# Performance work log

Measured on AMD Instinct MI355X. Metric: run time of the kernel, lower is better.

The kernel has to match this reference:

```python
import jax, jax.numpy as jnp
import numpy as np

B, S, D, H = 2, 2048, 2048, 16
HD = D // H            # 128
BLK = 16               # sparsity block size
LOCAL = 4              # num_local_blocks
GLOBAL = 1             # num_global_blocks
ROPE_THETA = 10000.0


def _fixed_layout(num_blocks: int) -> np.ndarray:
    """DeepSpeed FixedSparsityConfig block layout (unidirectional,
    different_layout_per_head=False, num_different_global_patterns=1,
    horizontal_global_attention=False)."""
    layout = np.zeros((num_blocks, num_blocks), dtype=bool)
    # local windows of LOCAL blocks, causal at block granularity inside window
    for w in range(0, num_blocks, LOCAL):
        end = min(w + LOCAL, num_blocks)
        for row in range(w, end):
            layout[row, w:row + 1] = True
    # vertical global columns: last GLOBAL block(s) of each window
    first = LOCAL - GLOBAL  # head % num_different_global_patterns == 0
    stop = num_blocks - (num_blocks % LOCAL)
    for i in range(first, stop, LOCAL):
        layout[i:, i:i + GLOBAL] = True  # unidirectional: rows >= i
    return layout

_LAYOUT = _fixed_layout(S // BLK)  # [num_blocks, num_blocks] bool, static


def _rope(t, cos, sin):
    # t: [B, S, H, HD]; pairs are adjacent (llama complex view)
    tr = t.reshape(B, S, H, HD // 2, 2)
    a, b = tr[..., 0], tr[..., 1]
    c = cos[None, :, None, :]
    s = sin[None, :, None, :]
    out = jnp.stack([a * c - b * s, a * s + b * c], axis=-1)
    return out.reshape(B, S, H, HD)


def setup_inputs() -> dict:
    key = jax.random.key(0)
    kx, kq, kk, kv, ko = jax.random.split(key, 5)
    x = jax.random.normal(kx, (B, S, D), dtype=jnp.float32)
    wscale = 1.0 / np.sqrt(D)
    wq = jax.random.normal(kq, (D, D), dtype=jnp.float32) * wscale
    wk = jax.random.normal(kk, (D, D), dtype=jnp.float32) * wscale
    wv = jax.random.normal(kv, (D, D), dtype=jnp.float32) * wscale
    wo = jax.random.normal(ko, (D, D), dtype=jnp.float32) * wscale
    # rotary tables (freqs_cis split into real/imag parts)
    freqs = 1.0 / (ROPE_THETA ** (np.arange(0, HD, 2, dtype=np.float32) / HD))
    angles = np.arange(S, dtype=np.float32)[:, None] * freqs[None, :]  # [S, HD//2]
    cos = jnp.asarray(np.cos(angles), dtype=jnp.float32)
    sin = jnp.asarray(np.sin(angles), dtype=jnp.float32)
    return {"x": x, "cos": cos, "sin": sin, "wq": wq, "wk": wk, "wv": wv, "wo": wo}


def reference(x, cos, sin, wq, wk, wv, wo):
    xq = (x @ wq).reshape(B, S, H, HD)
    xk = (x @ wk).reshape(B, S, H, HD)
    xv = (x @ wv).reshape(B, S, H, HD)
    xq = _rope(xq, cos, sin)
    xk = _rope(xk, cos, sin)
    # module casts q/k/v to fp16 before the sparse kernel; emulate precision
    xq = xq.astype(jnp.float16).astype(jnp.float32)
    xk = xk.astype(jnp.float16).astype(jnp.float32)
    xv = xv.astype(jnp.float16).astype(jnp.float32)
    q = jnp.transpose(xq, (0, 2, 1, 3))  # [B, H, S, HD]
    k = jnp.transpose(xk, (0, 2, 1, 3))
    v = jnp.transpose(xv, (0, 2, 1, 3))
    scale = 1.0 / np.sqrt(HD)
    scores = jnp.einsum('bhqd,bhkd->bhqk', q, k) * scale
    # block-granularity sparsity mask (DeepSpeed masks only at block level)
    blk = jnp.arange(S) // BLK
    mask = jnp.asarray(_LAYOUT)[blk[:, None], blk[None, :]]  # [S, S] bool
    scores = jnp.where(mask[None, None], scores, -jnp.inf)
    probs = jax.nn.softmax(scores, axis=-1)
    out = jnp.einsum('bhqk,bhkd->bhqd', probs, v)  # [B, H, S, HD]
    out = jnp.transpose(out, (0, 2, 1, 3)).reshape(B, S, D)
    return out @ wo
```

## Files before the change

### kernel.cpp

```cpp
#include <hip/hip_runtime.h>

#define B_ 2
#define S_ 2048
#define D_ 2048
#define H_ 16
#define HD_ 128

typedef _Float16 fp16x2 __attribute__((ext_vector_type(2)));
typedef _Float16 fp16x4 __attribute__((ext_vector_type(4)));
typedef _Float16 fp16x8 __attribute__((ext_vector_type(8)));
typedef float f32x4 __attribute__((ext_vector_type(4)));

__device__ __forceinline__ void gl_lds16(const _Float16* g, _Float16* l) {
  __builtin_amdgcn_global_load_lds((const __attribute__((address_space(1))) void*)g,
                                   (__attribute__((address_space(3))) void*)l, 16, 0, 0);
}

__global__ __launch_bounds__(256) void k_cast(const float* __restrict__ in,
                                              _Float16* __restrict__ out, int n4) {
  int i = blockIdx.x * 256 + threadIdx.x;
  if (i >= n4) return;
  f32x4 v = ((const f32x4*)in)[i];
  fp16x4 h = {(_Float16)v[0], (_Float16)v[1], (_Float16)v[2], (_Float16)v[3]};
  ((fp16x4*)out)[i] = h;
}

__global__ __launch_bounds__(256) void k_trw4(const float* __restrict__ w0,
                                              const float* __restrict__ w1,
                                              const float* __restrict__ w2,
                                              const float* __restrict__ w3,
                                              _Float16* __restrict__ o0,
                                              _Float16* __restrict__ o1,
                                              _Float16* __restrict__ o2,
                                              _Float16* __restrict__ o3) {
  __shared__ float tile[64][65];
  const float* w = (blockIdx.z == 0) ? w0 : (blockIdx.z == 1) ? w1 : (blockIdx.z == 2) ? w2 : w3;
  _Float16* wt = (blockIdx.z == 0) ? o0 : (blockIdx.z == 1) ? o1 : (blockIdx.z == 2) ? o2 : o3;
  int k0 = blockIdx.y * 64, n0 = blockIdx.x * 64;
  int t = threadIdx.x;
  int r = t >> 2, c0 = (t & 3) * 16;
  const float* ip = w + (size_t)(k0 + r) * D_ + n0 + c0;
#pragma unroll
  for (int j = 0; j < 16; j += 4) {
    f32x4 v = *(const f32x4*)(ip + j);
    tile[r][c0 + j] = v[0]; tile[r][c0 + j + 1] = v[1];
    tile[r][c0 + j + 2] = v[2]; tile[r][c0 + j + 3] = v[3];
  }
  __syncthreads();
  _Float16* op = wt + (size_t)(n0 + r) * D_ + k0 + c0;
#pragma unroll
  for (int j = 0; j < 16; j += 8) {
    fp16x8 v;
#pragma unroll
    for (int q = 0; q < 8; ++q) v[q] = (_Float16)tile[c0 + j + q][r];
    *(fp16x8*)(op + j) = v;
  }
}

__global__ __launch_bounds__(256, 4) void k_gemm_qkv(const _Float16* __restrict__ A,
                                                     const _Float16* __restrict__ BT,
                                                     const float* __restrict__ cosT,
                                                     const float* __restrict__ sinT,
                                                     _Float16* __restrict__ Qo,
                                                     _Float16* __restrict__ Ko,
                                                     _Float16* __restrict__ Vo) {
  __shared__ __align__(16) _Float16 lA[128 * 64];
  __shared__ __align__(16) _Float16 lB[128 * 64];
  const int t = threadIdx.x;
  const int fid = blockIdx.y * 48 + blockIdx.x;
  const int xcd = fid & 7, j = fid >> 3;
  const int m0 = (j / 6) * 128;
  const int n0 = (xcd * 6 + j % 6) * 128;
  const int lane = t & 63, w = t >> 6;
  const int l15 = lane & 15, lg = lane >> 4;
  const int wm = (w >> 1) * 64, wn = (w & 1) * 64;
  const int rs = t >> 3, cs = (t & 7) * 8;
  const _Float16* Ag = A + (size_t)(m0 + rs) * 2048 + cs;
  const _Float16* Bg = BT + (size_t)(n0 + rs) * 2048 + cs;
  _Float16* lAw = lA + w * 512;
  _Float16* lBw = lB + w * 512;
  f32x4 acc[4][4] = {};
  for (int k0 = 0; k0 < 2048; k0 += 64) {
#pragma unroll
    for (int i = 0; i < 4; ++i) {
      gl_lds16(Ag + k0 + (size_t)i * 32 * 2048, lAw + i * 2048);
      gl_lds16(Bg + k0 + (size_t)i * 32 * 2048, lBw + i * 2048);
    }
    __syncthreads();
#pragma unroll
    for (int ks = 0; ks < 2; ++ks) {
      const int ko = ks * 32 + 8 * lg;
      fp16x8 af[4], bf[4];
#pragma unroll
      for (int mi = 0; mi < 4; ++mi)
        af[mi] = *(const fp16x8*)&lA[(wm + mi * 16 + l15) * 64 + ko];
#pragma unroll
      for (int ni = 0; ni < 4; ++ni)
        bf[ni] = *(const fp16x8*)&lB[(wn + ni * 16 + l15) * 64 + ko];
#pragma unroll
      for (int mi = 0; mi < 4; ++mi)
#pragma unroll
        for (int ni = 0; ni < 4; ++ni)
          acc[mi][ni] = __builtin_amdgcn_mfma_f32_16x16x32_f16(af[mi], bf[ni], acc[mi][ni], 0, 0, 0);
    }
    __syncthreads();
  }

  const int region = n0 >> 11;
  if (region < 2) {
    _Float16* Out = (region == 0) ? Qo : Ko;
#pragma unroll
    for (int mi = 0; mi < 4; ++mi)
#pragma unroll
      for (int ni = 0; ni < 4; ++ni) {
        const int col = n0 + wn + 16 * ni + l15;
        const int d = col & 127;
        const int h = (col >> 7) & 15;
        const int dp = d >> 1;
        const bool odd = d & 1;
#pragma unroll
        for (int i = 0; i < 4; ++i) {
          const int row = m0 + wm + 16 * mi + 4 * lg + i;
          const int b = row >> 11, sl = row & 2047;
          const float self = acc[mi][ni][i];
          const float partner = __shfl_xor(self, 1);
          const float c = cosT[sl * 64 + dp], sn = sinT[sl * 64 + dp];
          const float val = odd ? (partner * sn + self * c) : (self * c - partner * sn);
          Out[(((size_t)b * H_ + h) * S_ + sl) * HD_ + d] = (_Float16)val;
        }
      }
  } else {
#pragma unroll
    for (int mi = 0; mi < 4; ++mi)
#pragma unroll
      for (int ni = 0; ni < 4; ++ni) {
        const int col = n0 + wn + 16 * ni + l15;
        const int d = col & 127;
        const int h = (col >> 7) & 15;
        const int row0 = m0 + wm + 16 * mi + 4 * lg;
        const int b = row0 >> 11, sl0 = row0 & 2047;
        const int kb = sl0 >> 4, kin = sl0 & 15;
        fp16x4 v4;
#pragma unroll
        for (int i = 0; i < 4; ++i) v4[i] = (_Float16)acc[mi][ni][i];
        *(fp16x4*)(Vo + ((((size_t)b * H_ + h) * 128 + kb) * 128 + d) * 16 + kin) = v4;
      }
  }
}

template <typename OUT>
__global__ __launch_bounds__(256) void k_gemm_bt(const _Float16* __restrict__ A,
                                                 const _Float16* __restrict__ BT,
                                                 OUT* __restrict__ C, int N) {
  __shared__ __align__(16) _Float16 lA[128 * 64];
  __shared__ __align__(16) _Float16 lB[128 * 64];
  const int t = threadIdx.x;
  const int fid = blockIdx.y * 16 + blockIdx.x;
  const int xcd = fid & 7, j = fid >> 3;
  const int m0 = (j >> 1) * 128;
  const int n0 = (xcd * 2 + (j & 1)) * 128;
  const int lane = t & 63, w = t >> 6;
  const int l15 = lane & 15, lg = lane >> 4;
  const int wm = (w >> 1) * 64, wn = (w & 1) * 64;
  const int rs = t >> 3, cs = (t & 7) * 8;
  const _Float16* Ag = A + (size_t)(m0 + rs) * 2048 + cs;
  const _Float16* Bg = BT + (size_t)(n0 + rs) * 2048 + cs;
  _Float16* lAw = lA + w * 512;
  _Float16* lBw = lB + w * 512;
  f32x4 acc[4][4] = {};
  for (int k0 = 0; k0 < 2048; k0 += 64) {
#pragma unroll
    for (int i = 0; i < 4; ++i) {
      gl_lds16(Ag + k0 + (size_t)i * 32 * 2048, lAw + i * 2048);
      gl_lds16(Bg + k0 + (size_t)i * 32 * 2048, lBw + i * 2048);
    }
    __syncthreads();
#pragma unroll
    for (int ks = 0; ks < 2; ++ks) {
      const int ko = ks * 32 + 8 * lg;
      fp16x8 af[4], bf[4];
#pragma unroll
      for (int mi = 0; mi < 4; ++mi)
        af[mi] = *(const fp16x8*)&lA[(wm + mi * 16 + l15) * 64 + ko];
#pragma unroll
      for (int ni = 0; ni < 4; ++ni)
        bf[ni] = *(const fp16x8*)&lB[(wn + ni * 16 + l15) * 64 + ko];
#pragma unroll
      for (int mi = 0; mi < 4; ++mi)
#pragma unroll
        for (int ni = 0; ni < 4; ++ni)
          acc[mi][ni] = __builtin_amdgcn_mfma_f32_16x16x32_f16(af[mi], bf[ni], acc[mi][ni], 0, 0, 0);
    }
    __syncthreads();
  }
#pragma unroll
  for (int mi = 0; mi < 4; ++mi)
#pragma unroll
    for (int ni = 0; ni < 4; ++ni) {
      size_t row = m0 + wm + 16 * mi + 4 * lg;
      size_t col = n0 + wn + 16 * ni + l15;
#pragma unroll
      for (int i = 0; i < 4; ++i)
        C[(row + i) * (size_t)N + col] = (OUT)acc[mi][ni][i];
    }
}

__global__ __launch_bounds__(256) void k_attn(const _Float16* __restrict__ Q,
                                              const _Float16* __restrict__ K,
                                              const _Float16* __restrict__ Vb,
                                              _Float16* __restrict__ Oa) {
  __shared__ __align__(16) _Float16 sK[2][2][2048];
  __shared__ __align__(16) _Float16 sV[2][2][2048];
  const int p = blockIdx.x;
  const int qgA = 31 - p, qgB = p;
  const int hh = blockIdx.y, b = blockIdx.z;
  const int t = threadIdx.x;
  const int w = t >> 6, lane = t & 63;
  const int l15 = lane & 15, lg = lane >> 4, g4 = lg * 4;
  const size_t bh = (size_t)b * H_ + hh;
  const float scale = 0.08838834764831845f;

  const int qbA = 4 * qgA + w, qbB = 4 * qgB + w;
  const int LA = qgA + 4, LB = qgB + 4;
  const int nchA = (LA + 1) >> 1, nchB = (LB + 1) >> 1;
  const int total = nchA + nchB;

  const _Float16* QpA = Q + (bh * S_ + (size_t)qbA * 16 + l15) * HD_ + lg * 8;
  const _Float16* QpB = Q + (bh * S_ + (size_t)qbB * 16 + l15) * HD_ + lg * 8;
  fp16x8 qfA[4], qfB[4];
#pragma unroll
  for (int dd = 0; dd < 4; ++dd) {
    qfA[dd] = *(const fp16x8*)(QpA + dd * 32);
    qfB[dd] = *(const fp16x8*)(QpB + dd * 32);
  }
  f32x4 o[8] = {};
  float mrun = -3.0e38f, lsum = 0.f;

  const int sr = t >> 4, sc = t & 15;
  const int ksrc_off = sr * 128 + (sc ^ (sr & 7)) * 8;
  const _Float16* Kb_g = K + bh * S_ * HD_;
  const _Float16* Vb_g = Vb + bh * (size_t)(128 * 2048);

  auto kbof = [&](int qg, int idx) { return idx < qg ? 4 * idx + 3 : 3 * qg + idx; };
  auto chunk_kbs = [&](int ci, int& kb0, int& kb1) {
    int qg, cil;
    if (ci < nchA) { qg = qgA; cil = ci; } else { qg = qgB; cil = ci - nchA; }
    const int L = qg + 4;
    const int i0 = 2 * cil, i1 = i0 + 1;
    kb0 = kbof(qg, i0);
    kb1 = (i1 < L) ? kbof(qg, i1) : kb0;
  };
  auto stage = [&](int buf, int ci) {
    int kb0, kb1;
    chunk_kbs(ci, kb0, kb1);
    gl_lds16(Kb_g + (size_t)kb0 * 2048 + ksrc_off, &sK[buf][0][w * 512]);
    gl_lds16(Kb_g + (size_t)kb1 * 2048 + ksrc_off, &sK[buf][1][w * 512]);
    gl_lds16(Vb_g + (size_t)kb0 * 2048 + t * 8, &sV[buf][0][w * 512]);
    gl_lds16(Vb_g + (size_t)kb1 * 2048 + t * 8, &sV[buf][1][w * 512]);
  };
  auto flush = [&](int qb) {
    const float inv = 1.f / lsum;
    f32x4 li;
#pragma unroll
    for (int i = 0; i < 4; ++i) li[i] = __shfl(inv, g4 + i);
    _Float16* Op = Oa + ((size_t)b * S_ + (size_t)qb * 16 + g4) * D_ + (size_t)hh * HD_ + l15;
#pragma unroll
    for (int ni = 0; ni < 8; ++ni)
#pragma unroll
      for (int i = 0; i < 4; ++i)
        Op[(size_t)i * D_ + 16 * ni] = (_Float16)(o[ni][i] * li[i]);
  };

  stage(0, 0);

  for (int ci = 0; ci < total; ++ci) {
    const int cur = ci & 1;
    if (ci == nchA) {
      flush(qbA);
#pragma unroll
      for (int ni = 0; ni < 8; ++ni) o[ni] = f32x4{0.f, 0.f, 0.f, 0.f};
      mrun = -3.0e38f;
      lsum = 0.f;
    }
    if (ci + 1 < total) {
      stage(cur ^ 1, ci + 1);
      asm volatile("s_waitcnt vmcnt(4)" ::: "memory");
    } else {
      asm volatile("s_waitcnt vmcnt(0)" ::: "memory");
    }
    __builtin_amdgcn_s_barrier();

    const bool inA = ci < nchA;
    const int qg = inA ? qgA : qgB;
    const int qb = inA ? qbA : qbB;
    const int cil = inA ? ci : ci - nchA;
    const int L = qg + 4;
    int kb0, kb1;
    chunk_kbs(ci, kb0, kb1);
    const bool v0 = kb0 <= qb;
    const bool v1 = (2 * cil + 1 < L) && (kb1 <= qb);
    f32x4 st[2];
    const float in0 = v0 ? 0.f : -1.0e30f, in1 = v1 ? 0.f : -1.0e30f;
    st[0] = f32x4{in0, in0, in0, in0};
    st[1] = f32x4{in1, in1, in1, in1};

    const char* kl = (const char*)&sK[cur][0][0];
    const int krow = l15 * 256;
#pragma unroll
    for (int dd = 0; dd < 4; ++dd) {
      const int co = ((dd * 4 + lg) ^ (l15 & 7)) * 16;
      fp16x8 k0 = *(const fp16x8*)(kl + krow + co);
      fp16x8 k1 = *(const fp16x8*)(kl + 4096 + krow + co);
      const fp16x8 qf = inA ? qfA[dd] : qfB[dd];
      st[0] = __builtin_amdgcn_mfma_f32_16x16x32_f16(k0, qf, st[0], 0, 0, 0);
      st[1] = __builtin_amdgcn_mfma_f32_16x16x32_f16(k1, qf, st[1], 0, 0, 0);
    }
    float bm = -3.0e38f;
#pragma unroll
    for (int j = 0; j < 2; ++j)
#pragma unroll
      for (int i = 0; i < 4; ++i) {
        st[j][i] *= scale;
        bm = fmaxf(bm, st[j][i]);
      }
    bm = fmaxf(bm, __shfl_xor(bm, 16));
    bm = fmaxf(bm, __shfl_xor(bm, 32));
    const float mnew = fmaxf(mrun, bm);
    const float corr = __expf(mrun - mnew);
    float pr[2][4];
    float ps = 0.f;
#pragma unroll
    for (int j = 0; j < 2; ++j)
#pragma unroll
      for (int i = 0; i < 4; ++i) {
        pr[j][i] = __expf(st[j][i] - mnew);
        ps += pr[j][i];
      }
    ps += __shfl_xor(ps, 16);
    ps += __shfl_xor(ps, 32);
    lsum = lsum * corr + ps;
    mrun = mnew;
    f32x4 c4;
#pragma unroll
    for (int i = 0; i < 4; ++i) c4[i] = __shfl(corr, g4 + i);
#pragma unroll
    for (int ni = 0; ni < 8; ++ni) {
      o[ni][0] *= c4[0]; o[ni][1] *= c4[1]; o[ni][2] *= c4[2]; o[ni][3] *= c4[3];
    }
    fp16x4 ph0 = {(_Float16)pr[0][0], (_Float16)pr[0][1], (_Float16)pr[0][2], (_Float16)pr[0][3]};
    fp16x4 ph1 = {(_Float16)pr[1][0], (_Float16)pr[1][1], (_Float16)pr[1][2], (_Float16)pr[1][3]};
    const char* vl = (const char*)&sV[cur][0][0];
#pragma unroll
    for (int ni = 0; ni < 8; ++ni) {
      const int vo = (16 * ni + l15) * 32 + g4 * 2;
      fp16x4 vv0 = *(const fp16x4*)(vl + vo);
      fp16x4 vv1 = *(const fp16x4*)(vl + 4096 + vo);
      o[ni] = __builtin_amdgcn_mfma_f32_16x16x16f16(ph0, vv0, o[ni], 0, 0, 0);
      o[ni] = __builtin_amdgcn_mfma_f32_16x16x16f16(ph1, vv1, o[ni], 0, 0, 0);
    }
    __builtin_amdgcn_s_barrier();
  }

  flush(qbB);
}

extern "C" void kernel_launch(void* const* d_in, const int* in_sizes, int n_in,
                              void* d_out, int out_size, void* d_ws, size_t ws_size,
                              hipStream_t stream) {
  const float* x = (const float*)d_in[0];
  const float* cosT = (const float*)d_in[1];
  const float* sinT = (const float*)d_in[2];
  const float* wq = (const float*)d_in[3];
  const float* wk = (const float*)d_in[4];
  const float* wv = (const float*)d_in[5];
  const float* wo = (const float*)d_in[6];
  float* out = (float*)d_out;
  char* ws = (char*)d_ws;

  _Float16* x16 = (_Float16*)(ws);
  _Float16* wtq = (_Float16*)(ws + (16ull << 20));
  _Float16* wtk = (_Float16*)(ws + (24ull << 20));
  _Float16* wtv = (_Float16*)(ws + (32ull << 20));
  _Float16* wto = (_Float16*)(ws + (40ull << 20));
  _Float16* Q16 = (_Float16*)(ws + (48ull << 20));
  _Float16* K16 = (_Float16*)(ws + (64ull << 20));
  _Float16* Vb16 = (_Float16*)(ws + (80ull << 20));

  k_cast<<<8192, 256, 0, stream>>>(x, x16, (B_ * S_ * D_) / 4);
  k_trw4<<<dim3(32, 32, 4), 256, 0, stream>>>(wq, wk, wv, wo, wtq, wtk, wtv, wto);

  k_gemm_qkv<<<dim3(48, 32), 256, 0, stream>>>(x16, wtq, cosT, sinT, Q16, K16, Vb16);

  _Float16* attn16 = x16;
  k_attn<<<dim3(16, H_, B_), 256, 0, stream>>>(Q16, K16, Vb16, attn16);

  dim3 gg(D_ / 128, (B_ * S_) / 128);
  k_gemm_bt<float><<<gg, 256, 0, stream>>>(attn16, wto, out, D_);
}
```

Baseline: 238.9 us.

## Rewrite QKV GEMM with 256x256 tiles, double-buffered LDS and swizzled layout

Rewrites the fused QKV projection GEMM to use 512-thread blocks computing 256x256 output tiles, with a two-stage LDS double buffer so the next K-slice is prefetched via global_load_lds while MFMAs run on the current one. LDS columns are XOR-swizzled to avoid bank conflicts, MFMA phases are wrapped in setprio, and the grid is remapped so consecutive tiles land on the same XCD. The goal is more data reuse per tile and overlap of memory loads with compute. The cost is 128 KB of LDS and higher register pressure, which limits occupancy to one block per CU, and the grid shrinks to 384 blocks.

```diff
diff --git a/kernel.cpp b/kernel.cpp
--- a/kernel.cpp
+++ b/kernel.cpp
@@ -57,60 +57,98 @@
   }
 }
 
-__global__ __launch_bounds__(256, 4) void k_gemm_qkv(const _Float16* __restrict__ A,
-                                                     const _Float16* __restrict__ BT,
-                                                     const float* __restrict__ cosT,
-                                                     const float* __restrict__ sinT,
-                                                     _Float16* __restrict__ Qo,
-                                                     _Float16* __restrict__ Ko,
-                                                     _Float16* __restrict__ Vo) {
-  __shared__ __align__(16) _Float16 lA[128 * 64];
-  __shared__ __align__(16) _Float16 lB[128 * 64];
-  const int t = threadIdx.x;
-  const int fid = blockIdx.y * 48 + blockIdx.x;
-  const int xcd = fid & 7, j = fid >> 3;
-  const int m0 = (j / 6) * 128;
-  const int n0 = (xcd * 6 + j % 6) * 128;
-  const int lane = t & 63, w = t >> 6;
+__global__ __launch_bounds__(512) void k_gemm_qkv(const _Float16* __restrict__ A,
+                                                  const _Float16* __restrict__ BT,
+                                                  const float* __restrict__ cosT,
+                                                  const float* __restrict__ sinT,
+                                                  _Float16* __restrict__ Qo,
+                                                  _Float16* __restrict__ Ko,
+                                                  _Float16* __restrict__ Vo) {
+  __shared__ __align__(16) _Float16 smem[65536];
+  const int tid = threadIdx.x;
+  const int w = tid >> 6, lane = tid & 63;
   const int l15 = lane & 15, lg = lane >> 4;
-  const int wm = (w >> 1) * 64, wn = (w & 1) * 64;
-  const int rs = t >> 3, cs = (t & 7) * 8;
-  const _Float16* Ag = A + (size_t)(m0 + rs) * 2048 + cs;
-  const _Float16* Bg = BT + (size_t)(n0 + rs) * 2048 + cs;
-  _Float16* lAw = lA + w * 512;
-  _Float16* lBw = lB + w * 512;
-  f32x4 acc[4][4] = {};
-  for (int k0 = 0; k0 < 2048; k0 += 64) {
-#pragma unroll
-    for (int i = 0; i < 4; ++i) {
-      gl_lds16(Ag + k0 + (size_t)i * 32 * 2048, lAw + i * 2048);
-      gl_lds16(Bg + k0 + (size_t)i * 32 * 2048, lBw + i * 2048);
-    }
-    __syncthreads();
-#pragma unroll
-    for (int ks = 0; ks < 2; ++ks) {
-      const int ko = ks * 32 + 8 * lg;
-      fp16x8 af[4], bf[4];
-#pragma unroll
-      for (int mi = 0; mi < 4; ++mi)
-        af[mi] = *(const fp16x8*)&lA[(wm + mi * 16 + l15) * 64 + ko];
-#pragma unroll
-      for (int ni = 0; ni < 4; ++ni)
-        bf[ni] = *(const fp16x8*)&lB[(wn + ni * 16 + l15) * 64 + ko];
-#pragma unroll
-      for (int mi = 0; mi < 4; ++mi)
-#pragma unroll
-        for (int ni = 0; ni < 4; ++ni)
-          acc[mi][ni] = __builtin_amdgcn_mfma_f32_16x16x32_f16(af[mi], bf[ni], acc[mi][ni], 0, 0, 0);
-    }
-    __syncthreads();
+  const int bid = blockIdx.x;
+  const int sid = (bid & 7) * 48 + (bid >> 3);
+  const int m0 = (sid & 15) * 256, n0 = (sid >> 4) * 256;
+  const int wm = (w >> 2) * 128, wn = (w & 3) * 64;
+  const int lr = lane >> 3, lc = lane & 7;
+  const int scol = ((lc ^ lr) << 3);
+  const _Float16* Arow = A + (size_t)(m0 + w * 8 + lr) * 2048 + scol;
+  const _Float16* Brow = BT + (size_t)(n0 + w * 8 + lr) * 2048 + scol;
+  _Float16* dA = smem + w * 512;
+  _Float16* dB = smem + 32768 + w * 512;
+
+  auto stageA = [&](int stg, int h, int ss, int k0) {
+    gl_lds16(Arow + (size_t)(h * 128 + ss * 64) * 2048 + k0,
+             dA + stg * 16384 + h * 8192 + ss * 4096);
+  };
+  auto stageB = [&](int stg, int h, int ss, int k0) {
+    gl_lds16(Brow + (size_t)(h * 128 + ss * 64) * 2048 + k0,
+             dB + stg * 16384 + h * 8192 + ss * 4096);
+  };
+
+  f32x4 acc[8][4] = {};
+
+  stageA(0, 0, 0, 0); stageA(0, 0, 1, 0); stageA(0, 1, 0, 0); stageA(0, 1, 1, 0);
+  stageB(0, 0, 0, 0); stageB(0, 0, 1, 0); stageB(0, 1, 0, 0); stageB(0, 1, 1, 0);
+  asm volatile("s_waitcnt vmcnt(0)" ::: "memory");
+  __builtin_amdgcn_s_barrier();
+
+  for (int t = 0; t < 32; ++t) {
+    const int cur = t & 1, stg = cur ^ 1;
+    const int k1 = (t + 1) * 64;
+    const bool more = (t + 1) < 32;
+#pragma unroll
+    for (int p = 0; p < 4; ++p) {
+      if (p == 0 && more) {
+        stageA(stg, 0, 0, k1); stageA(stg, 0, 1, k1);
+        stageA(stg, 1, 0, k1); stageA(stg, 1, 1, k1);
+      }
+      if (p == 1 && more) {
+        stageB(stg, 0, 0, k1); stageB(stg, 0, 1, k1);
+        stageB(stg, 1, 0, k1); stageB(stg, 1, 1, k1);
+      }
+      const int qm = p >> 1, qn = p & 1;
+      fp16x8 af[4][2], bf[2][2];
+#pragma unroll
+      for (int mi2 = 0; mi2 < 4; ++mi2)
+#pragma unroll
+        for (int ks = 0; ks < 2; ++ks) {
+          const int row = qm * 64 + mi2 * 16 + l15;
+          af[mi2][ks] = *(const fp16x8*)(smem + cur * 16384 + (w >> 2) * 8192 + row * 64 +
+                                         ((ks * 32 + lg * 8) ^ ((l15 & 7) * 8)));
+        }
+#pragma unroll
+      for (int ni2 = 0; ni2 < 2; ++ni2)
+#pragma unroll
+        for (int ks = 0; ks < 2; ++ks) {
+          const int rb = wn + (qn * 2 + ni2) * 16 + l15;
+          bf[ni2][ks] = *(const fp16x8*)(smem + 32768 + cur * 16384 + (rb >> 7) * 8192 +
+                                         (rb & 127) * 64 + ((ks * 32 + lg * 8) ^ ((l15 & 7) * 8)));
+        }
+      asm volatile("s_waitcnt lgkmcnt(0)" ::: "memory");
+      __builtin_amdgcn_sched_barrier(0);
+      __builtin_amdgcn_s_setprio(1);
+#pragma unroll
+      for (int mi2 = 0; mi2 < 4; ++mi2)
+#pragma unroll
+        for (int ni2 = 0; ni2 < 2; ++ni2)
+#pragma unroll
+          for (int ks = 0; ks < 2; ++ks)
+            acc[qm * 4 + mi2][qn * 2 + ni2] = __builtin_amdgcn_mfma_f32_16x16x32_f16(
+                af[mi2][ks], bf[ni2][ks], acc[qm * 4 + mi2][qn * 2 + ni2], 0, 0, 0);
+      __builtin_amdgcn_s_setprio(0);
+      if (p == 3) asm volatile("s_waitcnt vmcnt(0)" ::: "memory");
+      __builtin_amdgcn_s_barrier();
+    }
   }
 
   const int region = n0 >> 11;
   if (region < 2) {
     _Float16* Out = (region == 0) ? Qo : Ko;
 #pragma unroll
-    for (int mi = 0; mi < 4; ++mi)
+    for (int mi = 0; mi < 8; ++mi)
 #pragma unroll
       for (int ni = 0; ni < 4; ++ni) {
         const int col = n0 + wn + 16 * ni + l15;
@@ -131,7 +169,7 @@
       }
   } else {
 #pragma unroll
-    for (int mi = 0; mi < 4; ++mi)
+    for (int mi = 0; mi < 8; ++mi)
 #pragma unroll
       for (int ni = 0; ni < 4; ++ni) {
         const int col = n0 + wn + 16 * ni + l15;
@@ -389,7 +427,7 @@
   k_cast<<<8192, 256, 0, stream>>>(x, x16, (B_ * S_ * D_) / 4);
   k_trw4<<<dim3(32, 32, 4), 256, 0, stream>>>(wq, wk, wv, wo, wtq, wtk, wtv, wto);
 
-  k_gemm_qkv<<<dim3(48, 32), 256, 0, stream>>>(x16, wtq, cosT, sinT, Q16, K16, Vb16);
+  k_gemm_qkv<<<384, 512, 0, stream>>>(x16, wtq, cosT, sinT, Q16, K16, Vb16);
 
   _Float16* attn16 = x16;
   k_attn<<<dim3(16, H_, B_), 256, 0, stream>>>(Q16, K16, Vb16, attn16);
```

Result: slower. 252.7 us (+5.8%).

## Replace GEMMs with double-buffered 256x128 tile kernel using swizzled LDS

Applied to the files above, without the earlier changes.

Both projection GEMMs now run through one templated kernel with 512 threads and 256x128 output tiles. It double-buffers LDS tiles, prefetching the next K-slice with global_load_lds and waiting with a partial vmcnt, so memory loads overlap the MFMA work. An XOR swizzle on LDS columns is meant to avoid bank conflicts, and s_setprio raises priority around the MFMA block. The trade-off is 96KB of LDS per block, which limits occupancy, and fewer blocks in the grid.

```diff
diff --git a/kernel.cpp b/kernel.cpp
--- a/kernel.cpp
+++ b/kernel.cpp
@@ -57,152 +57,142 @@
   }
 }
 
-__global__ __launch_bounds__(256, 4) void k_gemm_qkv(const _Float16* __restrict__ A,
-                                                     const _Float16* __restrict__ BT,
-                                                     const float* __restrict__ cosT,
-                                                     const float* __restrict__ sinT,
-                                                     _Float16* __restrict__ Qo,
-                                                     _Float16* __restrict__ Ko,
-                                                     _Float16* __restrict__ Vo) {
-  __shared__ __align__(16) _Float16 lA[128 * 64];
-  __shared__ __align__(16) _Float16 lB[128 * 64];
-  const int t = threadIdx.x;
-  const int fid = blockIdx.y * 48 + blockIdx.x;
-  const int xcd = fid & 7, j = fid >> 3;
-  const int m0 = (j / 6) * 128;
-  const int n0 = (xcd * 6 + j % 6) * 128;
-  const int lane = t & 63, w = t >> 6;
+template <int MODE>
+__global__ __launch_bounds__(512) void k_gemm256(const _Float16* __restrict__ A,
+                                                 const _Float16* __restrict__ BT,
+                                                 const float* __restrict__ cosT,
+                                                 const float* __restrict__ sinT,
+                                                 _Float16* __restrict__ Qo,
+                                                 _Float16* __restrict__ Ko,
+                                                 _Float16* __restrict__ Vo,
+                                                 float* __restrict__ Cf) {
+  __shared__ __align__(16) _Float16 smem[49152];
+  const int tid = threadIdx.x;
+  const int w = tid >> 6, lane = tid & 63;
   const int l15 = lane & 15, lg = lane >> 4;
-  const int wm = (w >> 1) * 64, wn = (w & 1) * 64;
-  const int rs = t >> 3, cs = (t & 7) * 8;
-  const _Float16* Ag = A + (size_t)(m0 + rs) * 2048 + cs;
-  const _Float16* Bg = BT + (size_t)(n0 + rs) * 2048 + cs;
-  _Float16* lAw = lA + w * 512;
-  _Float16* lBw = lB + w * 512;
+  const int NPX = (MODE == 0) ? 6 : 2;
+  const int bid = blockIdx.x;
+  const int xcd = bid & 7, j = bid >> 3;
+  const int m0 = (j / NPX) * 256;
+  const int n0 = (xcd * NPX + j % NPX) * 128;
+  const int wm = (w >> 1) * 64;
+  const int wn = (w & 1) * 64;
+  const int lr = lane >> 3, lc = lane & 7;
+  const int scol = (lc ^ lr) << 3;
+  const _Float16* Asrc = A + (size_t)(m0 + w * 8 + lr) * 2048 + scol;
+  const _Float16* Bsrc = BT + (size_t)(n0 + w * 8 + lr) * 2048 + scol;
+  _Float16* dstA = smem + w * 512;
+  _Float16* dstB = smem + 32768 + w * 512;
+
+  auto stageA = [&](int stg, int u, int k0) {
+    gl_lds16(Asrc + (size_t)u * 64 * 2048 + k0, dstA + stg * 16384 + u * 4096);
+  };
+  auto stageB = [&](int stg, int u, int k0) {
+    gl_lds16(Bsrc + (size_t)u * 64 * 2048 + k0, dstB + stg * 8192 + u * 4096);
+  };
+
   f32x4 acc[4][4] = {};
-  for (int k0 = 0; k0 < 2048; k0 += 64) {
-#pragma unroll
-    for (int i = 0; i < 4; ++i) {
-      gl_lds16(Ag + k0 + (size_t)i * 32 * 2048, lAw + i * 2048);
-      gl_lds16(Bg + k0 + (size_t)i * 32 * 2048, lBw + i * 2048);
-    }
-    __syncthreads();
-#pragma unroll
-    for (int ks = 0; ks < 2; ++ks) {
-      const int ko = ks * 32 + 8 * lg;
-      fp16x8 af[4], bf[4];
+
+#pragma unroll
+  for (int u = 0; u < 4; ++u) stageA(0, u, 0);
+  stageB(0, 0, 0); stageB(0, 1, 0);
+
+  for (int t = 0; t < 32; ++t) {
+    const int cur = t & 1, stg = cur ^ 1;
+    if (t + 1 < 32) {
+      const int k1 = (t + 1) * 64;
+#pragma unroll
+      for (int u = 0; u < 4; ++u) stageA(stg, u, k1);
+      stageB(stg, 0, k1); stageB(stg, 1, k1);
+      asm volatile("s_waitcnt vmcnt(6)" ::: "memory");
+    } else {
+      asm volatile("s_waitcnt vmcnt(0)" ::: "memory");
+    }
+    __builtin_amdgcn_s_barrier();
+
+    fp16x8 af[4][2], bf[4][2];
+#pragma unroll
+    for (int mi = 0; mi < 4; ++mi)
+#pragma unroll
+      for (int ks = 0; ks < 2; ++ks) {
+        const int row = wm + mi * 16 + l15;
+        af[mi][ks] = *(const fp16x8*)(smem + cur * 16384 + (row >> 6) * 4096 +
+                                      (row & 63) * 64 + ((ks * 32 + lg * 8) ^ ((l15 & 7) * 8)));
+      }
+#pragma unroll
+    for (int ni = 0; ni < 4; ++ni)
+#pragma unroll
+      for (int ks = 0; ks < 2; ++ks) {
+        const int row = wn + ni * 16 + l15;
+        bf[ni][ks] = *(const fp16x8*)(smem + 32768 + cur * 8192 + (row >> 6) * 4096 +
+                                      (row & 63) * 64 + ((ks * 32 + lg * 8) ^ ((l15 & 7) * 8)));
+      }
+    __builtin_amdgcn_s_setprio(1);
+#pragma unroll
+    for (int mi = 0; mi < 4; ++mi)
+#pragma unroll
+      for (int ni = 0; ni < 4; ++ni)
+#pragma unroll
+        for (int ks = 0; ks < 2; ++ks)
+          acc[mi][ni] = __builtin_amdgcn_mfma_f32_16x16x32_f16(af[mi][ks], bf[ni][ks],
+                                                               acc[mi][ni], 0, 0, 0);
+    __builtin_amdgcn_s_setprio(0);
+    __builtin_amdgcn_s_barrier();
+  }
+
+  if (MODE == 0) {
+    const int region = n0 >> 11;
+    if (region < 2) {
+      _Float16* Out = (region == 0) ? Qo : Ko;
 #pragma unroll
       for (int mi = 0; mi < 4; ++mi)
-        af[mi] = *(const fp16x8*)&lA[(wm + mi * 16 + l15) * 64 + ko];
-#pragma unroll
-      for (int ni = 0; ni < 4; ++ni)
-        bf[ni] = *(const fp16x8*)&lB[(wn + ni * 16 + l15) * 64 + ko];
+#pragma unroll
+        for (int ni = 0; ni < 4; ++ni) {
+          const int col = n0 + wn + 16 * ni + l15;
+          const int d = col & 127;
+          const int h = (col >> 7) & 15;
+          const int dp = d >> 1;
+          const bool odd = d & 1;
+#pragma unroll
+          for (int i = 0; i < 4; ++i) {
+            const int row = m0 + wm + 16 * mi + 4 * lg + i;
+            const int b = row >> 11, sl = row & 2047;
+            const float self = acc[mi][ni][i];
+            const float partner = __shfl_xor(self, 1);
+            const float c = cosT[sl * 64 + dp], sn = sinT[sl * 64 + dp];
+            const float val = odd ? (partner * sn + self * c) : (self * c - partner * sn);
+            Out[(((size_t)b * H_ + h) * S_ + sl) * HD_ + d] = (_Float16)val;
+          }
+        }
+    } else {
 #pragma unroll
       for (int mi = 0; mi < 4; ++mi)
 #pragma unroll
-        for (int ni = 0; ni < 4; ++ni)
-          acc[mi][ni] = __builtin_amdgcn_mfma_f32_16x16x32_f16(af[mi], bf[ni], acc[mi][ni], 0, 0, 0);
-    }
-    __syncthreads();
-  }
-
-  const int region = n0 >> 11;
-  if (region < 2) {
-    _Float16* Out = (region == 0) ? Qo : Ko;
+        for (int ni = 0; ni < 4; ++ni) {
+          const int col = n0 + wn + 16 * ni + l15;
+          const int d = col & 127;
+          const int h = (col >> 7) & 15;
+          const int row0 = m0 + wm + 16 * mi + 4 * lg;
+          const int b = row0 >> 11, sl0 = row0 & 2047;
+          const int kb = sl0 >> 4, kin = sl0 & 15;
+          fp16x4 v4;
+#pragma unroll
+          for (int i = 0; i < 4; ++i) v4[i] = (_Float16)acc[mi][ni][i];
+          *(fp16x4*)(Vo + ((((size_t)b * H_ + h) * 128 + kb) * 128 + d) * 16 + kin) = v4;
+        }
+    }
+  } else {
 #pragma unroll
     for (int mi = 0; mi < 4; ++mi)
 #pragma unroll
       for (int ni = 0; ni < 4; ++ni) {
-        const int col = n0 + wn + 16 * ni + l15;
-        const int d = col & 127;
-        const int h = (col >> 7) & 15;
-        const int dp = d >> 1;
-        const bool odd = d & 1;
-#pragma unroll
-        for (int i = 0; i < 4; ++i) {
-          const int row = m0 + wm + 16 * mi + 4 * lg + i;
-          const int b = row >> 11, sl = row & 2047;
-          const float self = acc[mi][ni][i];
-          const float partner = __shfl_xor(self, 1);
-          const float c = cosT[sl * 64 + dp], sn = sinT[sl * 64 + dp];
-          const float val = odd ? (partner * sn + self * c) : (self * c - partner * sn);
-          Out[(((size_t)b * H_ + h) * S_ + sl) * HD_ + d] = (_Float16)val;
-        }
-      }
-  } else {
-#pragma unroll
-    for (int mi = 0; mi < 4; ++mi)
-#pragma unroll
-      for (int ni = 0; ni < 4; ++ni) {
-        const int col = n0 + wn + 16 * ni + l15;
-        const int d = col & 127;
-        const int h = (col >> 7) & 15;
-        const int row0 = m0 + wm + 16 * mi + 4 * lg;
-        const int b = row0 >> 11, sl0 = row0 & 2047;
-        const int kb = sl0 >> 4, kin = sl0 & 15;
-        fp16x4 v4;
-#pragma unroll
-        for (int i = 0; i < 4; ++i) v4[i] = (_Float16)acc[mi][ni][i];
-        *(fp16x4*)(Vo + ((((size_t)b * H_ + h) * 128 + kb) * 128 + d) * 16 + kin) = v4;
-      }
-  }
-}
-
-template <typename OUT>
-__global__ __launch_bounds__(256) void k_gemm_bt(const _Float16* __restrict__ A,
-                                                 const _Float16* __restrict__ BT,
-                                                 OUT* __restrict__ C, int N) {
-  __shared__ __align__(16) _Float16 lA[128 * 64];
-  __shared__ __align__(16) _Float16 lB[128 * 64];
-  const int t = threadIdx.x;
-  const int fid = blockIdx.y * 16 + blockIdx.x;
-  const int xcd = fid & 7, j = fid >> 3;
-  const int m0 = (j >> 1) * 128;
-  const int n0 = (xcd * 2 + (j & 1)) * 128;
-  const int lane = t & 63, w = t >> 6;
-  const int l15 = lane & 15, lg = lane >> 4;
-  const int wm = (w >> 1) * 64, wn = (w & 1) * 64;
-  const int rs = t >> 3, cs = (t & 7) * 8;
-  const _Float16* Ag = A + (size_t)(m0 + rs) * 2048 + cs;
-  const _Float16* Bg = BT + (size_t)(n0 + rs) * 2048 + cs;
-  _Float16* lAw = lA + w * 512;
-  _Float16* lBw = lB + w * 512;
-  f32x4 acc[4][4] = {};
-  for (int k0 = 0; k0 < 2048; k0 += 64) {
-#pragma unroll
-    for (int i = 0; i < 4; ++i) {
-      gl_lds16(Ag + k0 + (size_t)i * 32 * 2048, lAw + i * 2048);
-      gl_lds16(Bg + k0 + (size_t)i * 32 * 2048, lBw + i * 2048);
-    }
-    __syncthreads();
-#pragma unroll
-    for (int ks = 0; ks < 2; ++ks) {
-      const int ko = ks * 32 + 8 * lg;
-      fp16x8 af[4], bf[4];
-#pragma unroll
-      for (int mi = 0; mi < 4; ++mi)
-        af[mi] = *(const fp16x8*)&lA[(wm + mi * 16 + l15) * 64 + ko];
-#pragma unroll
-      for (int ni = 0; ni < 4; ++ni)
-        bf[ni] = *(const fp16x8*)&lB[(wn + ni * 16 + l15) * 64 + ko];
-#pragma unroll
-      for (int mi = 0; mi < 4; ++mi)
-#pragma unroll
-        for (int ni = 0; ni < 4; ++ni)
-          acc[mi][ni] = __builtin_amdgcn_mfma_f32_16x16x32_f16(af[mi], bf[ni], acc[mi][ni], 0, 0, 0);
-    }
-    __syncthreads();
-  }
-#pragma unroll
-  for (int mi = 0; mi < 4; ++mi)
-#pragma unroll
-    for (int ni = 0; ni < 4; ++ni) {
-      size_t row = m0 + wm + 16 * mi + 4 * lg;
-      size_t col = n0 + wn + 16 * ni + l15;
-#pragma unroll
-      for (int i = 0; i < 4; ++i)
-        C[(row + i) * (size_t)N + col] = (OUT)acc[mi][ni][i];
-    }
+        const size_t row = m0 + wm + 16 * mi + 4 * lg;
+        const size_t col = n0 + wn + 16 * ni + l15;
+#pragma unroll
+        for (int i = 0; i < 4; ++i)
+          Cf[(row + i) * 2048 + col] = acc[mi][ni][i];
+      }
+  }
 }
 
 __global__ __launch_bounds__(256) void k_attn(const _Float16* __restrict__ Q,
@@ -389,11 +379,11 @@
   k_cast<<<8192, 256, 0, stream>>>(x, x16, (B_ * S_ * D_) / 4);
   k_trw4<<<dim3(32, 32, 4), 256, 0, stream>>>(wq, wk, wv, wo, wtq, wtk, wtv, wto);
 
-  k_gemm_qkv<<<dim3(48, 32), 256, 0, stream>>>(x16, wtq, cosT, sinT, Q16, K16, Vb16);
+  k_gemm256<0><<<768, 512, 0, stream>>>(x16, wtq, cosT, sinT, Q16, K16, Vb16, nullptr);
 
   _Float16* attn16 = x16;
   k_attn<<<dim3(16, H_, B_), 256, 0, stream>>>(Q16, K16, Vb16, attn16);
 
-  dim3 gg(D_ / 128, (B_ * S_) / 128);
-  k_gemm_bt<float><<<gg, 256, 0, stream>>>(attn16, wto, out, D_);
-}
+  k_gemm256<1><<<256, 512, 0, stream>>>(attn16, wto, nullptr, nullptr, nullptr, nullptr,
+                                        nullptr, out);
+}
```

Result: faster. 221.7 us (median of 2 runs) (-7.2%).
